# Performance work log

Hardware: AMD Instinct MI355X
Metric: run time of the kernel (lower is better)

## Reference

```python
import jax, jax.numpy as jnp
import numpy as np

H = 16        # num query heads
H_KV = 4      # num kv heads
D = 128       # head_dim
ROPE_BASE = 10000.0


def rotate_half(x):
    x1, x2 = jnp.split(x, 2, axis=-1)
    return jnp.concatenate((-x2, x1), axis=-1)


def rope_tables(T, d, dtype):
    inv_freq = 1.0 / (ROPE_BASE ** (np.arange(0, d, 2, dtype=np.float32) / d))
    t = np.arange(T, dtype=np.float32)
    freqs = np.outer(t, inv_freq)                 # [T, d/2]
    emb = np.concatenate((freqs, freqs), axis=-1)  # [T, d]
    return jnp.asarray(np.cos(emb), dtype), jnp.asarray(np.sin(emb), dtype)


def setup_inputs() -> dict:
    key = jax.random.key(0)
    ks = jax.random.split(key, 5)
    B, T, C = 2, 2048, 2048
    s = 0.02
    return {
        "x": jax.random.normal(ks[0], (B, T, C), jnp.float32),
        "wq": jax.random.normal(ks[1], (C, H * D), jnp.float32) * s,
        "wk": jax.random.normal(ks[2], (C, H_KV * D), jnp.float32) * s,
        "wv": jax.random.normal(ks[3], (C, H_KV * D), jnp.float32) * s,
        "wo": jax.random.normal(ks[4], (H * D, C), jnp.float32) * s,
    }


def reference(x, wq, wk, wv, wo):
    B, T, C = x.shape
    # QKV projections (bias=False); weights stored as [in, out]
    q = (x @ wq).reshape(B, T, H, D).transpose(0, 2, 1, 3)      # [B,H,T,D]
    k = (x @ wk).reshape(B, T, H_KV, D).transpose(0, 2, 1, 3)   # [B,Hkv,T,D]
    v = (x @ wv).reshape(B, T, H_KV, D).transpose(0, 2, 1, 3)
    # RoPE
    cos, sin = rope_tables(T, D, x.dtype)                        # [T,D]
    q = q * cos + rotate_half(q) * sin
    k = k * cos + rotate_half(k) * sin
    # GQA: repeat kv heads
    n_rep = H // H_KV
    k = jnp.repeat(k, n_rep, axis=1)                             # [B,H,T,D]
    v = jnp.repeat(v, n_rep, axis=1)
    # Causal SDPA
    scale = 1.0 / jnp.sqrt(jnp.asarray(D, x.dtype))
    att = jnp.einsum('bhqd,bhkd->bhqk', q, k) * scale            # [B,H,T,T]
    causal = jnp.tril(jnp.ones((T, T), dtype=bool))
    att = jnp.where(causal, att, jnp.asarray(-jnp.inf, x.dtype))
    att = jax.nn.softmax(att, axis=-1)
    y = jnp.einsum('bhqk,bhkd->bhqd', att, v)                    # [B,H,T,D]
    y = y.transpose(0, 2, 1, 3).reshape(B, T, H * D)
    return y @ wo
```

## Files before the change

kernel.cpp:

```cpp
#include <hip/hip_runtime.h>
#include <cstdint>
#include <cstddef>

typedef __attribute__((ext_vector_type(8))) short short8;
typedef __attribute__((ext_vector_type(4))) float f4;
typedef __attribute__((ext_vector_type(4))) unsigned int u4;

static __device__ __forceinline__ unsigned short f2bf(float x) {
  unsigned int u = __float_as_uint(x);
  unsigned int r = (u + 0x7FFFu + ((u >> 16) & 1u)) >> 16;
  return (unsigned short)r;
}

static __device__ __forceinline__ void gll16(const unsigned short* g, unsigned short* l) {
  __builtin_amdgcn_global_load_lds(
      (const __attribute__((address_space(1))) unsigned int*)g,
      (__attribute__((address_space(3))) unsigned int*)l, 16, 0, 0);
}

template <int N>
static __device__ __forceinline__ void wait_vmcnt() {
  if constexpr (N == 0) asm volatile("s_waitcnt vmcnt(0)" ::: "memory");
  else if constexpr (N == 1) asm volatile("s_waitcnt vmcnt(1)" ::: "memory");
  else if constexpr (N == 2) asm volatile("s_waitcnt vmcnt(2)" ::: "memory");
  else if constexpr (N == 3) asm volatile("s_waitcnt vmcnt(3)" ::: "memory");
  else if constexpr (N == 4) asm volatile("s_waitcnt vmcnt(4)" ::: "memory");
}

static __device__ __forceinline__ void trans_tile(
    const float* __restrict__ src, unsigned short* __restrict__ dst,
    int R, int C, int c0, int r0, int tid, unsigned short* tile) {
#pragma unroll
  for (int s = 0; s < 2; ++s) {
    int chunk = tid + s * 256;
    int c8 = chunk & 7, r = chunk >> 3;
    const float* p = src + (size_t)(r0 + r) * C + c0 + c8 * 8;
    f4 a = *(const f4*)p;
    f4 b = *(const f4*)(p + 4);
    union { unsigned short u[8]; u4 v; } pk;
#pragma unroll
    for (int i = 0; i < 4; ++i) { pk.u[i] = f2bf(a[i]); pk.u[4 + i] = f2bf(b[i]); }
    *(u4*)(tile + r * 72 + c8 * 8) = pk.v;
  }
  __syncthreads();
#pragma unroll
  for (int s = 0; s < 2; ++s) {
    int chunk = tid + s * 256;
    int r8 = chunk & 7, c = chunk >> 3;
    union { unsigned short u[8]; u4 v; } pk;
#pragma unroll
    for (int i = 0; i < 8; ++i) pk.u[i] = tile[(r8 * 8 + i) * 72 + c];
    *(u4*)(dst + (size_t)(c0 + c) * R + r0 + r8 * 8) = pk.v;
  }
}

__global__ __launch_bounds__(256) void k_prep(
    const float* __restrict__ x, const float* __restrict__ wq,
    const float* __restrict__ wk, const float* __restrict__ wv,
    unsigned short* __restrict__ Xb, unsigned short* __restrict__ WqkvT) {
  __shared__ alignas(16) unsigned short tile[64 * 72];
  int bid = blockIdx.x;
  int tid = threadIdx.x;
  if (bid < 4096) {
    int gid = bid * 256 + tid;
    const float* p = x + (size_t)gid * 8;
    f4 a = *(const f4*)p;
    f4 b = *(const f4*)(p + 4);
    union { unsigned short u[8]; u4 v; } pk;
#pragma unroll
    for (int i = 0; i < 4; ++i) { pk.u[i] = f2bf(a[i]); pk.u[4 + i] = f2bf(b[i]); }
    *(u4*)(Xb + (size_t)gid * 8) = pk.v;
  } else if (bid < 4096 + 1024) {
    int idx = bid - 4096;
    trans_tile(wq, WqkvT, 2048, 2048, (idx & 31) * 64, (idx >> 5) * 64, tid, tile);
  } else if (bid < 4096 + 1024 + 256) {
    int idx = bid - (4096 + 1024);
    trans_tile(wk, WqkvT + (size_t)2048 * 2048, 2048, 512,
               (idx & 7) * 64, (idx >> 3) * 64, tid, tile);
  } else {
    int idx = bid - (4096 + 1024 + 256);
    trans_tile(wv, WqkvT + (size_t)2560 * 2048, 2048, 512,
               (idx & 7) * 64, (idx >> 3) * 64, tid, tile);
  }
}

__global__ __launch_bounds__(256) void k_transpose_f(
    const float* __restrict__ src, unsigned short* __restrict__ dst, int R, int C) {
  __shared__ alignas(16) unsigned short tile[64 * 72];
  trans_tile(src, dst, R, C, blockIdx.x * 64, blockIdx.y * 64, threadIdx.x, tile);
}

#define PHASE(QM, QN, WAITC, ...)                                              \
  {                                                                            \
    wait_vmcnt<WAITC>();                                                       \
    __builtin_amdgcn_s_barrier();                                              \
    asm volatile("" ::: "memory");                                             \
    short8 af[FI][2], bf[2][2];                                                \
    _Pragma("unroll") for (int i = 0; i < FI; ++i)                             \
      _Pragma("unroll") for (int ks = 0; ks < 2; ++ks)                         \
        af[i][ks] = *(const short8*)(&As[cur][((QM) * (BM / 2) + wm * (BM / 4) + i * 16 + l16) * 64 + kswz[ks]]); \
    _Pragma("unroll") for (int j = 0; j < 2; ++j)                              \
      _Pragma("unroll") for (int ks = 0; ks < 2; ++ks)                         \
        bf[j][ks] = *(const short8*)(&Bs[cur][((QN) * 128 + wn * 32 + j * 16 + l16) * 64 + kswz[ks]]); \
    __VA_ARGS__                                                                \
    __builtin_amdgcn_s_setprio(1);                                             \
    _Pragma("unroll") for (int i = 0; i < FI; ++i)                             \
      _Pragma("unroll") for (int j = 0; j < 2; ++j)                            \
        _Pragma("unroll") for (int ks = 0; ks < 2; ++ks)                       \
          acc[(QM) * FI + i][(QN) * 2 + j] = __builtin_amdgcn_mfma_f32_16x16x32_bf16( \
              af[i][ks], bf[j][ks], acc[(QM) * FI + i][(QN) * 2 + j], 0, 0, 0); \
    __builtin_amdgcn_s_setprio(0);                                             \
  }

template <int BM, bool BF16OUT>
__global__ __launch_bounds__(512, 2) void k_gemm8(
    const unsigned short* __restrict__ A, const unsigned short* __restrict__ Bt,
    void* __restrict__ Cout, int M, int N, int K) {
  constexpr int CA = BM / 128;
  constexpr int FI = BM / 64;
  constexpr int WA = 2 + CA, WB = 2 * CA, WC = CA + 2, PB = CA;
  __shared__ alignas(16) unsigned short As[2][BM * 64];
  __shared__ alignas(16) unsigned short Bs[2][256 * 64];
  (void)M;

  int tid = threadIdx.x;
  int wid = tid >> 6, lane = tid & 63, quad = lane >> 4, l16 = lane & 15;
  int wm = wid >> 2, wn = wid & 3;

  int nx = gridDim.x;
  int id = blockIdx.y * nx + blockIdx.x;
  int nwg = nx * gridDim.y;
  int per = nwg >> 3;
  int lin = (id & 7) * per + (id >> 3);
  int bx = lin % nx, by = lin / nx;
  int bm = by * BM, bn = bx * 256;

  int srow = lane >> 3;
  int scol = ((lane & 7) ^ srow) << 3;
  const unsigned short* Ast = A + (size_t)(bm + wid * 8 + srow) * K + scol;
  const unsigned short* Bst = Bt + (size_t)(bn + wid * 8 + srow) * K + scol;
  const int ldsw = wid * 512;

  int kswz[2];
#pragma unroll
  for (int ks = 0; ks < 2; ++ks) kswz[ks] = (ks * 32 + quad * 8) ^ ((l16 & 7) << 3);

  f4 zero = {0.f, 0.f, 0.f, 0.f};
  f4 acc[2 * FI][4];
#pragma unroll
  for (int i = 0; i < 2 * FI; ++i)
#pragma unroll
    for (int j = 0; j < 4; ++j) acc[i][j] = zero;

  if constexpr (CA == 2) {
    gll16(Ast, &As[0][ldsw]);
    gll16(Ast + (size_t)64 * K, &As[0][ldsw + 64 * 64]);
  } else {
    gll16(Ast, &As[0][ldsw]);
  }
  gll16(Bst, &Bs[0][ldsw]);
  gll16(Bst + (size_t)64 * K, &Bs[0][ldsw + 64 * 64]);
  gll16(Bst + (size_t)128 * K, &Bs[0][ldsw + 128 * 64]);
  gll16(Bst + (size_t)192 * K, &Bs[0][ldsw + 192 * 64]);
  if constexpr (CA == 2) {
    gll16(Ast + (size_t)128 * K, &As[0][ldsw + 128 * 64]);
    gll16(Ast + (size_t)192 * K, &As[0][ldsw + 192 * 64]);
  } else {
    gll16(Ast + (size_t)64 * K, &As[0][ldsw + 64 * 64]);
  }

  int nt = K >> 6;
  int cur = 0;
  for (int t = 0; t < nt - 1; ++t) {
    int k0n = (t + 1) << 6;
    int nxt = cur ^ 1;
    unsigned short* Asn = &As[nxt][0];
    unsigned short* Bsn = &Bs[nxt][0];
    PHASE(0, 0, WA,
      if constexpr (CA == 2) {
        gll16(Ast + k0n, Asn + ldsw);
        gll16(Ast + (size_t)64 * K + k0n, Asn + ldsw + 64 * 64);
      } else {
        gll16(Ast + k0n, Asn + ldsw);
      })
    PHASE(0, 1, WB,
      gll16(Bst + k0n, Bsn + ldsw);
      gll16(Bst + (size_t)64 * K + k0n, Bsn + ldsw + 64 * 64);)
    PHASE(1, 0, WC,
      gll16(Bst + (size_t)128 * K + k0n, Bsn + ldsw + 128 * 64);
      gll16(Bst + (size_t)192 * K + k0n, Bsn + ldsw + 192 * 64);)
    PHASE(1, 1, -1,
      if constexpr (CA == 2) {
        gll16(Ast + (size_t)128 * K + k0n, Asn + ldsw + 128 * 64);
        gll16(Ast + (size_t)192 * K + k0n, Asn + ldsw + 192 * 64);
      } else {
        gll16(Ast + (size_t)64 * K + k0n, Asn + ldsw + 64 * 64);
      })
    cur = nxt;
  }
  PHASE(0, 0, WA, ;)
  PHASE(0, 1, PB, ;)
  PHASE(1, 0, 0, ;)
  PHASE(1, 1, -1, ;)

#pragma unroll
  for (int mi = 0; mi < 2 * FI; ++mi) {
    int row = bm + (mi / FI) * (BM / 2) + wm * (BM / 4) + (mi % FI) * 16 + quad * 4;
#pragma unroll
    for (int nj = 0; nj < 4; ++nj) {
      int col = bn + (nj >> 1) * 128 + wn * 32 + (nj & 1) * 16 + l16;
#pragma unroll
      for (int r = 0; r < 4; ++r) {
        if constexpr (BF16OUT)
          ((unsigned short*)Cout)[(size_t)(row + r) * N + col] = f2bf(acc[mi][nj][r]);
        else
          ((float*)Cout)[(size_t)(row + r) * N + col] = acc[mi][nj][r];
      }
    }
  }
}

__global__ __launch_bounds__(256) void k_ropev(
    unsigned short* __restrict__ QKV, unsigned short* __restrict__ VT) {
  __shared__ alignas(16) unsigned short tile[64 * 72];
  int bid = blockIdx.x;
  int tid = threadIdx.x;
  if (bid < 512) {
    int gid = bid * 256 + tid;
    int c8 = gid & 7; int g = gid >> 3;
    int h4 = g & 3; g >>= 2;
    int t = g & 2047; int b = g >> 11;
    size_t p = (size_t)(b * 2048 + t) * 3072 + 2048 + h4 * 128 + c8 * 8;
    short8 x0 = *(const short8*)(QKV + p);
    short8 x1 = *(const short8*)(QKV + p + 64);
    short8 o0, o1;
    float tf = (float)t;
#pragma unroll
    for (int i = 0; i < 8; ++i) {
      int d = c8 * 8 + i;
      float a0 = __uint_as_float((unsigned int)(unsigned short)x0[i] << 16);
      float a1 = __uint_as_float((unsigned int)(unsigned short)x1[i] << 16);
      float freq = exp2f(-(float)d * 0.20762050593046f);
      float ang = tf * freq;
      float cv = __cosf(ang), sv = __sinf(ang);
      o0[i] = (short)f2bf(a0 * cv - a1 * sv);
      o1[i] = (short)f2bf(a1 * cv + a0 * sv);
    }
    *(short8*)(QKV + p) = o0;
    *(short8*)(QKV + p + 64) = o1;
  } else {
    int idx = bid - 512;
    int t0 = (idx & 31) * 64;
    int g = idx >> 5;
    int dh = g & 1, hk = (g >> 1) & 3, b = g >> 3;
    int d0 = dh * 64;
    const unsigned short* src = QKV + (size_t)(b * 2048 + t0) * 3072 + 2560 + hk * 128 + d0;
#pragma unroll
    for (int s = 0; s < 2; ++s) {
      int chunk = tid + s * 256;
      int c8 = chunk & 7, r = chunk >> 3;
      *(u4*)(tile + r * 72 + c8 * 8) = *(const u4*)(src + (size_t)r * 3072 + c8 * 8);
    }
    __syncthreads();
    unsigned short* dst = VT + ((size_t)((b * 4 + hk) * 128 + d0)) * 2048 + t0;
#pragma unroll
    for (int s = 0; s < 2; ++s) {
      int chunk = tid + s * 256;
      int r8 = chunk & 7, c = chunk >> 3;
      union { unsigned short u[8]; u4 v; } pk;
#pragma unroll
      for (int i = 0; i < 8; ++i) pk.u[i] = tile[(r8 * 8 + i) * 72 + c];
      *(u4*)(dst + (size_t)c * 2048 + r8 * 8) = pk.v;
    }
  }
}

static __device__ __forceinline__ void attn_step(
    const unsigned short* __restrict__ Ks, const unsigned short* __restrict__ Vs,
    const short8* qf, f4* o, float& m, float& l,
    int quad, int l16, int qrow, int K0, bool mask, bool odd) {
  f4 zero = {0.f, 0.f, 0.f, 0.f};
  f4 st[4];
  __builtin_amdgcn_s_setprio(1);
#pragma unroll
  for (int kt = 0; kt < 4; ++kt) {
    st[kt] = zero;
#pragma unroll
    for (int ks = 0; ks < 4; ++ks) {
      short8 kf = *(const short8*)(Ks + (kt * 16 + l16) * 136 + ks * 32 + quad * 8);
      st[kt] = __builtin_amdgcn_mfma_f32_16x16x32_bf16(kf, qf[ks], st[kt], 0, 0, 0);
    }
  }
  __builtin_amdgcn_s_setprio(0);
  if (mask) {
#pragma unroll
    for (int kt = 0; kt < 4; ++kt)
#pragma unroll
      for (int r = 0; r < 4; ++r)
        if (K0 + kt * 16 + quad * 4 + r > qrow) st[kt][r] = -1e30f;
  }
  float sm = -1e30f;
#pragma unroll
  for (int kt = 0; kt < 4; ++kt)
#pragma unroll
    for (int r = 0; r < 4; ++r) sm = fmaxf(sm, st[kt][r]);
  sm = fmaxf(sm, __shfl_xor(sm, 16));
  sm = fmaxf(sm, __shfl_xor(sm, 32));
  bool grow = !__all(sm - m <= 8.f);
  float mnew = grow ? fmaxf(m, sm) : m;
  f4 pv[4];
  float rs = 0.f;
#pragma unroll
  for (int kt = 0; kt < 4; ++kt)
#pragma unroll
    for (int r = 0; r < 4; ++r) {
      pv[kt][r] = __expf(st[kt][r] - mnew);
      rs += pv[kt][r];
    }
  rs += __shfl_xor(rs, 16);
  rs += __shfl_xor(rs, 32);
  if (grow) {
    float alpha = __expf(m - mnew);
    l = l * alpha + rs;
    m = mnew;
#pragma unroll
    for (int i = 0; i < 8; ++i) o[i] *= alpha;
  } else {
    l += rs;
  }
  unsigned int c[4][2];
#pragma unroll
  for (int kt = 0; kt < 4; ++kt)
#pragma unroll
    for (int p = 0; p < 2; ++p)
      asm("v_cvt_pk_bf16_f32 %0, %1, %2"
          : "=v"(c[kt][p]) : "v"(pv[kt][2 * p]), "v"(pv[kt][2 * p + 1]));
#pragma unroll
  for (int kh = 0; kh < 2; ++kh) {
    unsigned int A0 = c[2 * kh][0], A1 = c[2 * kh][1];
    unsigned int B0 = c[2 * kh + 1][0], B1 = c[2 * kh + 1][1];
    asm("v_permlane32_swap_b32 %0, %1" : "+v"(A0), "+v"(B0));
    asm("v_permlane32_swap_b32 %0, %1" : "+v"(A1), "+v"(B1));
    unsigned int tA0 = (unsigned int)__builtin_amdgcn_ds_swizzle((int)A0, 0x401F);
    unsigned int tA1 = (unsigned int)__builtin_amdgcn_ds_swizzle((int)A1, 0x401F);
    unsigned int tB0 = (unsigned int)__builtin_amdgcn_ds_swizzle((int)B0, 0x401F);
    unsigned int tB1 = (unsigned int)__builtin_amdgcn_ds_swizzle((int)B1, 0x401F);
    union { unsigned int u[4]; short8 s; } pb;
    pb.u[0] = odd ? tB0 : A0;
    pb.u[1] = odd ? tB1 : A1;
    pb.u[2] = odd ? B0 : tA0;
    pb.u[3] = odd ? B1 : tA1;
    __builtin_amdgcn_s_setprio(1);
#pragma unroll
    for (int i = 0; i < 8; ++i) {
      short8 vf = *(const short8*)(Vs + (i * 16 + l16) * 72 + kh * 32 + quad * 8);
      o[i] = __builtin_amdgcn_mfma_f32_16x16x32_bf16(vf, pb.s, o[i], 0, 0, 0);
    }
    __builtin_amdgcn_s_setprio(0);
  }
}

__global__ __launch_bounds__(256, 2) void k_attn(
    const unsigned short* __restrict__ QKV,
    const unsigned short* __restrict__ VT,
    unsigned short* __restrict__ Y) {
  __shared__ alignas(16) unsigned short Ks[2][64 * 136];
  __shared__ alignas(16) unsigned short Vs[128 * 72];
  int tid = threadIdx.x;
  int w = tid >> 6, lane = tid & 63, quad = lane >> 4, l16 = lane & 15;
  bool odd = (quad & 1) != 0;
  int bh = blockIdx.y; int b = bh >> 4, h = bh & 15, hk = h >> 2;
  int v = blockIdx.x;
  int q0A = v * 64 + w * 16;
  int q0B = (31 - v) * 64 + w * 16;
  const unsigned short* Qh = QKV + (size_t)b * 2048 * 3072 + h * 128;
  const unsigned short* Kh = QKV + (size_t)b * 2048 * 3072 + 2048 + hk * 128;
  const unsigned short* Vh = VT + ((size_t)(b * 4 + hk) * 128) * 2048;

  int rK0 = tid >> 4, cK = tid & 15;
  int rV0 = tid >> 3, cV = tid & 7;

  short8 qfA[4], qfB[4];
#pragma unroll
  for (int ks = 0; ks < 4; ++ks) {
    qfA[ks] = *(const short8*)(Qh + (size_t)(q0A + l16) * 3072 + ks * 32 + quad * 8);
    qfB[ks] = *(const short8*)(Qh + (size_t)(q0B + l16) * 3072 + ks * 32 + quad * 8);
  }
#pragma unroll
  for (int tix = 0; tix < 2; ++tix) {
    short8* qf = tix ? qfB : qfA;
    float tf = (float)((tix ? q0B : q0A) + l16);
#pragma unroll
    for (int ks = 0; ks < 2; ++ks)
#pragma unroll
      for (int i = 0; i < 8; ++i) {
        int d = ks * 32 + quad * 8 + i;
        float x0 = __uint_as_float((unsigned int)(unsigned short)qf[ks][i] << 16);
        float x1 = __uint_as_float((unsigned int)(unsigned short)qf[ks + 2][i] << 16);
        float freq = exp2f(-(float)d * 0.20762050593046f);
        float ang = tf * freq;
        float cv = __cosf(ang), sv = __sinf(ang);
        qf[ks][i] = (short)f2bf((x0 * cv - x1 * sv) * 0.088388347648318f);
        qf[ks + 2][i] = (short)f2bf((x1 * cv + x0 * sv) * 0.088388347648318f);
      }
  }

  f4 zero = {0.f, 0.f, 0.f, 0.f};
  f4 oA[8], oB[8];
#pragma unroll
  for (int i = 0; i < 8; ++i) { oA[i] = zero; oB[i] = zero; }
  float mA = -1e30f, lA = 0.f, mB = -1e30f, lB = 0.f;

  int nch = 32 - v;

#pragma unroll
  for (int s = 0; s < 4; ++s) {
    int rK = rK0 + 16 * s;
    *(u4*)(&Ks[0][0] + rK * 136 + cK * 8) =
        *(const u4*)(Kh + (size_t)rK * 3072 + cK * 8);
    int rV = rV0 + 32 * s;
    *(u4*)(Vs + rV * 72 + cV * 8) =
        *(const u4*)(Vh + (size_t)rV * 2048 + cV * 8);
  }
  __syncthreads();

  for (int kc = 0; kc < nch; ++kc) {
    int cur = kc & 1, nxt = cur ^ 1;
    int K0 = kc * 64;
    bool have_next = (kc + 1) < nch;
    u4 kreg[4], vreg[4];
    if (have_next) {
      int K0n = K0 + 64;
#pragma unroll
      for (int s = 0; s < 4; ++s) {
        int rK = rK0 + 16 * s;
        kreg[s] = *(const u4*)(Kh + (size_t)(K0n + rK) * 3072 + cK * 8);
        int rV = rV0 + 32 * s;
        vreg[s] = *(const u4*)(Vh + (size_t)rV * 2048 + K0n + cV * 8);
      }
    }

    if (kc <= v)
      attn_step(&Ks[cur][0], Vs, qfA, oA, mA, lA, quad, l16, q0A + l16, K0, kc == v, odd);
    attn_step(&Ks[cur][0], Vs, qfB, oB, mB, lB, quad, l16, q0B + l16, K0, kc == nch - 1, odd);

    if (have_next) {
#pragma unroll
      for (int s = 0; s < 4; ++s) {
        int rK = rK0 + 16 * s;
        *(u4*)(&Ks[nxt][0] + rK * 136 + cK * 8) = kreg[s];
      }
      __syncthreads();
#pragma unroll
      for (int s = 0; s < 4; ++s) {
        int rV = rV0 + 32 * s;
        *(u4*)(Vs + rV * 72 + cV * 8) = vreg[s];
      }
    }
    __syncthreads();
  }

  float rA = 1.f / lA, rB = 1.f / lB;
  size_t yrowA = (size_t)(b * 2048 + q0A + l16) * 2048 + h * 128;
  size_t yrowB = (size_t)(b * 2048 + q0B + l16) * 2048 + h * 128;
#pragma unroll
  for (int i = 0; i < 8; ++i)
#pragma unroll
    for (int r = 0; r < 4; ++r) {
      Y[yrowA + i * 16 + quad * 4 + r] = f2bf(oA[i][r] * rA);
      Y[yrowB + i * 16 + quad * 4 + r] = f2bf(oB[i][r] * rB);
    }
}

extern "C" void kernel_launch(void* const* d_in, const int* in_sizes, int n_in,
                              void* d_out, int out_size, void* d_ws, size_t ws_size,
                              hipStream_t stream) {
  const float* x  = (const float*)d_in[0];
  const float* wq = (const float*)d_in[1];
  const float* wk = (const float*)d_in[2];
  const float* wv = (const float*)d_in[3];
  const float* wo = (const float*)d_in[4];
  float* outp = (float*)d_out;

  unsigned short* WqkvT = (unsigned short*)d_out;
  unsigned short* VT    = WqkvT + (size_t)3072 * 2048;
  unsigned short* Xb    = VT + (size_t)2 * 4 * 128 * 2048;
  unsigned short* QKV = (unsigned short*)d_ws;
  unsigned short* Yb  = QKV + (size_t)4096 * 3072;
  unsigned short* WoT = QKV;

  dim3 blk(256);
  k_prep<<<dim3(5632), blk, 0, stream>>>(x, wq, wk, wv, Xb, WqkvT);

  k_gemm8<256, true><<<dim3(12, 16), dim3(512), 0, stream>>>(
      Xb, WqkvT, QKV, 4096, 3072, 2048);

  k_ropev<<<dim3(1024), blk, 0, stream>>>(QKV, VT);

  k_attn<<<dim3(16, 32), blk, 0, stream>>>(QKV, VT, Yb);

  k_transpose_f<<<dim3(32, 32), blk, 0, stream>>>(wo, WoT, 2048, 2048);
  k_gemm8<128, false><<<dim3(8, 32), dim3(512), 0, stream>>>(
      Yb, WoT, outp, 4096, 2048, 2048);
}
```

Before: 294.4 us.

## Replace paired causal q-tiles with one tile per block, heaviest first

New measurement: 352.8 us. +19.8%, slower.

```diff
diff --git a/kernel.cpp b/kernel.cpp
--- a/kernel.cpp
+++ b/kernel.cpp
@@ -370,9 +370,8 @@
   int w = tid >> 6, lane = tid & 63, quad = lane >> 4, l16 = lane & 15;
   bool odd = (quad & 1) != 0;
   int bh = blockIdx.y; int b = bh >> 4, h = bh & 15, hk = h >> 2;
-  int v = blockIdx.x;
-  int q0A = v * 64 + w * 16;
-  int q0B = (31 - v) * 64 + w * 16;
+  int v = 31 - blockIdx.x;
+  int q0 = v * 64 + w * 16;
   const unsigned short* Qh = QKV + (size_t)b * 2048 * 3072 + h * 128;
   const unsigned short* Kh = QKV + (size_t)b * 2048 * 3072 + 2048 + hk * 128;
   const unsigned short* Vh = VT + ((size_t)(b * 4 + hk) * 128) * 2048;
@@ -380,16 +379,12 @@
   int rK0 = tid >> 4, cK = tid & 15;
   int rV0 = tid >> 3, cV = tid & 7;
 
-  short8 qfA[4], qfB[4];
-#pragma unroll
-  for (int ks = 0; ks < 4; ++ks) {
-    qfA[ks] = *(const short8*)(Qh + (size_t)(q0A + l16) * 3072 + ks * 32 + quad * 8);
-    qfB[ks] = *(const short8*)(Qh + (size_t)(q0B + l16) * 3072 + ks * 32 + quad * 8);
-  }
-#pragma unroll
-  for (int tix = 0; tix < 2; ++tix) {
-    short8* qf = tix ? qfB : qfA;
-    float tf = (float)((tix ? q0B : q0A) + l16);
+  short8 qf[4];
+#pragma unroll
+  for (int ks = 0; ks < 4; ++ks)
+    qf[ks] = *(const short8*)(Qh + (size_t)(q0 + l16) * 3072 + ks * 32 + quad * 8);
+  {
+    float tf = (float)(q0 + l16);
 #pragma unroll
     for (int ks = 0; ks < 2; ++ks)
 #pragma unroll
@@ -406,12 +401,12 @@
   }
 
   f4 zero = {0.f, 0.f, 0.f, 0.f};
-  f4 oA[8], oB[8];
-#pragma unroll
-  for (int i = 0; i < 8; ++i) { oA[i] = zero; oB[i] = zero; }
-  float mA = -1e30f, lA = 0.f, mB = -1e30f, lB = 0.f;
-
-  int nch = 32 - v;
+  f4 o[8];
+#pragma unroll
+  for (int i = 0; i < 8; ++i) o[i] = zero;
+  float m = -1e30f, l = 0.f;
+
+  int nch = v + 1;
 
 #pragma unroll
   for (int s = 0; s < 4; ++s) {
@@ -440,9 +435,7 @@
       }
     }
 
-    if (kc <= v)
-      attn_step(&Ks[cur][0], Vs, qfA, oA, mA, lA, quad, l16, q0A + l16, K0, kc == v, odd);
-    attn_step(&Ks[cur][0], Vs, qfB, oB, mB, lB, quad, l16, q0B + l16, K0, kc == nch - 1, odd);
+    attn_step(&Ks[cur][0], Vs, qf, o, m, l, quad, l16, q0 + l16, K0, kc == v, odd);
 
     if (have_next) {
 #pragma unroll
@@ -460,16 +453,13 @@
     __syncthreads();
   }
 
-  float rA = 1.f / lA, rB = 1.f / lB;
-  size_t yrowA = (size_t)(b * 2048 + q0A + l16) * 2048 + h * 128;
-  size_t yrowB = (size_t)(b * 2048 + q0B + l16) * 2048 + h * 128;
+  float rl = 1.f / l;
+  size_t yrow = (size_t)(b * 2048 + q0 + l16) * 2048 + h * 128;
 #pragma unroll
   for (int i = 0; i < 8; ++i)
 #pragma unroll
-    for (int r = 0; r < 4; ++r) {
-      Y[yrowA + i * 16 + quad * 4 + r] = f2bf(oA[i][r] * rA);
-      Y[yrowB + i * 16 + quad * 4 + r] = f2bf(oB[i][r] * rB);
-    }
+    for (int r = 0; r < 4; ++r)
+      Y[yrow + i * 16 + quad * 4 + r] = f2bf(o[i][r] * rl);
 }
 
 extern "C" void kernel_launch(void* const* d_in, const int* in_sizes, int n_in,
@@ -497,7 +487,7 @@
 
   k_ropev<<<dim3(1024), blk, 0, stream>>>(QKV, VT);
 
-  k_attn<<<dim3(16, 32), blk, 0, stream>>>(QKV, VT, Yb);
+  k_attn<<<dim3(32, 32), blk, 0, stream>>>(QKV, VT, Yb);
 
   k_transpose_f<<<dim3(32, 32), blk, 0, stream>>>(wo, WoT, 2048, 2048);
   k_gemm8<128, false><<<dim3(8, 32), dim3(512), 0, stream>>>(
```
